# Optimization experiments

Measured on AMD Instinct MI355X. Metric: run time of the kernel, lower is better.

The kernel has to match this reference:

```python
import jax, jax.numpy as jnp
import numpy as np

D, N = 512, 65536


def setup_inputs() -> dict:
    key = jax.random.key(0)
    k1, k2 = jax.random.split(key)
    feats = jax.random.normal(k1, (D, N), dtype=jnp.float32)
    warped_feats = jax.random.normal(k2, (D, N), dtype=jnp.float32)
    return {"feats": feats, "warped_feats": warped_feats}


def reference(feats, warped_feats):
    # diag(feats.T @ warped_feats)[n] == sum_d feats[d,n] * warped_feats[d,n]
    # Same math as the torch module, without materializing the NxN matrix.
    diag = jnp.einsum('dn,dn->n', feats, warped_feats)  # [N]
    cosine = 1.0 - diag
    return cosine.mean()
```

## Files before the change

### kernel.cpp

```cpp
#include <hip/hip_runtime.h>

#define THREADS 256
#define GRID 2048

__global__ void zero_ws_kernel(float* ws) {
    ws[0] = 0.0f;
}

__global__ __launch_bounds__(THREADS) void dot_reduce_kernel(
        const float4* __restrict__ a,
        const float4* __restrict__ b,
        float* __restrict__ ws,
        long long n4) {
    long long idx    = (long long)blockIdx.x * THREADS + threadIdx.x;
    long long stride = (long long)gridDim.x * THREADS;

    float acc = 0.0f;
    for (long long i = idx; i < n4; i += stride) {
        float4 x = a[i];
        float4 y = b[i];
        acc = fmaf(x.x, y.x, acc);
        acc = fmaf(x.y, y.y, acc);
        acc = fmaf(x.z, y.z, acc);
        acc = fmaf(x.w, y.w, acc);
    }

    #pragma unroll
    for (int off = 32; off > 0; off >>= 1)
        acc += __shfl_down(acc, off, 64);

    __shared__ float smem[THREADS / 64];
    int lane = threadIdx.x & 63;
    int wave = threadIdx.x >> 6;
    if (lane == 0) smem[wave] = acc;
    __syncthreads();

    if (threadIdx.x == 0) {
        float s = 0.0f;
        #pragma unroll
        for (int w = 0; w < THREADS / 64; ++w) s += smem[w];
        atomicAdd(ws, s);
    }
}

__global__ void finalize_kernel(const float* __restrict__ ws,
                                float* __restrict__ out,
                                float inv_n) {
    out[0] = 1.0f - ws[0] * inv_n;
}

extern "C" void kernel_launch(void* const* d_in, const int* in_sizes, int n_in,
                              void* d_out, int out_size, void* d_ws, size_t ws_size,
                              hipStream_t stream) {
    const float* feats  = (const float*)d_in[0];
    const float* warped = (const float*)d_in[1];
    float* out = (float*)d_out;
    float* ws  = (float*)d_ws;

    const long long total = (long long)in_sizes[0];
    const long long n4 = total / 4;
    const float inv_n = 1.0f / 65536.0f;

    zero_ws_kernel<<<1, 1, 0, stream>>>(ws);
    dot_reduce_kernel<<<GRID, THREADS, 0, stream>>>(
        (const float4*)feats, (const float4*)warped, ws, n4);
    finalize_kernel<<<1, 1, 0, stream>>>(ws, out, inv_n);
}
```

Before: 281.9 us.

## Replace grid-stride atomic reduction with one-shot blocks and two-pass reduce

Result: no change. 276.8 us (-1.8%).

```diff
diff --git a/kernel.cpp b/kernel.cpp
--- a/kernel.cpp
+++ b/kernel.cpp
@@ -1,52 +1,71 @@
 #include <hip/hip_runtime.h>
 
 #define THREADS 256
-#define GRID 2048
+#define VPT 4
 
-__global__ void zero_ws_kernel(float* ws) {
-    ws[0] = 0.0f;
-}
-
-__global__ __launch_bounds__(THREADS) void dot_reduce_kernel(
+__global__ __launch_bounds__(THREADS) void dot_partial_kernel(
         const float4* __restrict__ a,
         const float4* __restrict__ b,
-        float* __restrict__ ws,
-        long long n4) {
-    long long idx    = (long long)blockIdx.x * THREADS + threadIdx.x;
-    long long stride = (long long)gridDim.x * THREADS;
+        float* __restrict__ partial) {
+    const int base = blockIdx.x * (THREADS * VPT) + threadIdx.x;
 
-    float acc = 0.0f;
-    for (long long i = idx; i < n4; i += stride) {
-        float4 x = a[i];
-        float4 y = b[i];
-        acc = fmaf(x.x, y.x, acc);
-        acc = fmaf(x.y, y.y, acc);
-        acc = fmaf(x.z, y.z, acc);
-        acc = fmaf(x.w, y.w, acc);
+    float4 xa[VPT], xb[VPT];
+    #pragma unroll
+    for (int j = 0; j < VPT; ++j) xa[j] = a[base + j * THREADS];
+    #pragma unroll
+    for (int j = 0; j < VPT; ++j) xb[j] = b[base + j * THREADS];
+
+    float acc[VPT];
+    #pragma unroll
+    for (int j = 0; j < VPT; ++j) {
+        acc[j] = xa[j].x * xb[j].x;
+        acc[j] = fmaf(xa[j].y, xb[j].y, acc[j]);
+        acc[j] = fmaf(xa[j].z, xb[j].z, acc[j]);
+        acc[j] = fmaf(xa[j].w, xb[j].w, acc[j]);
     }
+    float s = (acc[0] + acc[1]) + (acc[2] + acc[3]);
 
     #pragma unroll
     for (int off = 32; off > 0; off >>= 1)
-        acc += __shfl_down(acc, off, 64);
+        s += __shfl_down(s, off, 64);
 
     __shared__ float smem[THREADS / 64];
     int lane = threadIdx.x & 63;
     int wave = threadIdx.x >> 6;
-    if (lane == 0) smem[wave] = acc;
+    if (lane == 0) smem[wave] = s;
     __syncthreads();
 
     if (threadIdx.x == 0) {
-        float s = 0.0f;
+        float t = 0.f;
         #pragma unroll
-        for (int w = 0; w < THREADS / 64; ++w) s += smem[w];
-        atomicAdd(ws, s);
+        for (int w = 0; w < THREADS / 64; ++w) t += smem[w];
+        partial[blockIdx.x] = t;
     }
 }
 
-__global__ void finalize_kernel(const float* __restrict__ ws,
-                                float* __restrict__ out,
-                                float inv_n) {
-    out[0] = 1.0f - ws[0] * inv_n;
+__global__ __launch_bounds__(THREADS) void final_reduce_kernel(
+        const float* __restrict__ partial,
+        float* __restrict__ out,
+        int np, float inv_n) {
+    float s = 0.f;
+    for (int i = threadIdx.x; i < np; i += THREADS) s += partial[i];
+
+    #pragma unroll
+    for (int off = 32; off > 0; off >>= 1)
+        s += __shfl_down(s, off, 64);
+
+    __shared__ float smem[THREADS / 64];
+    int lane = threadIdx.x & 63;
+    int wave = threadIdx.x >> 6;
+    if (lane == 0) smem[wave] = s;
+    __syncthreads();
+
+    if (threadIdx.x == 0) {
+        float t = 0.f;
+        #pragma unroll
+        for (int w = 0; w < THREADS / 64; ++w) t += smem[w];
+        out[0] = 1.0f - t * inv_n;
+    }
 }
 
 extern "C" void kernel_launch(void* const* d_in, const int* in_sizes, int n_in,
@@ -58,11 +77,11 @@
     float* ws  = (float*)d_ws;
 
     const long long total = (long long)in_sizes[0];
-    const long long n4 = total / 4;
+    const int n4 = (int)(total / 4);
+    const int blocks = n4 / (THREADS * VPT);
     const float inv_n = 1.0f / 65536.0f;
 
-    zero_ws_kernel<<<1, 1, 0, stream>>>(ws);
-    dot_reduce_kernel<<<GRID, THREADS, 0, stream>>>(
-        (const float4*)feats, (const float4*)warped, ws, n4);
-    finalize_kernel<<<1, 1, 0, stream>>>(ws, out, inv_n);
+    dot_partial_kernel<<<blocks, THREADS, 0, stream>>>(
+        (const float4*)feats, (const float4*)warped, ws);
+    final_reduce_kernel<<<1, THREADS, 0, stream>>>(ws, out, blocks, inv_n);
 }
```
